# Kernel optimization log

Hardware: AMD Instinct MI355X
Metric: run time of the kernel (lower is better)

The kernel has to match this reference:

```python
import jax, jax.numpy as jnp
import numpy as np

KS = 3          # image feature patch kernel size
RATE = 2        # downsample rate; alpha patches use kernel RATE*2, stride RATE
PENALTY = -10000.0
EPS = 1e-4
BN_EPS = 1e-5


def _pad(x, k, s):
    # reflect 'same' padding as in GCAModule.pad
    l = (k - s + 1) // 2
    r = (k - s) // 2
    return jnp.pad(x, ((0, 0), (0, 0), (l, r), (l, r)), mode='reflect')


def _extract_patches(x, k, s):
    # replicates reflect-pad + F.unfold + reshape -> (n, L, c, k, k)
    x = _pad(x, k, s)
    n, c, H, W = x.shape
    oh = (H - k) // s + 1
    ow = (W - k) // s + 1
    cols = [x[:, :, di:di + s * (oh - 1) + 1:s, dj:dj + s * (ow - 1) + 1:s]
            for di in range(k) for dj in range(k)]
    p = jnp.stack(cols, axis=2).reshape(n, c, k, k, oh * ow)  # (n,c,k,k,L)
    return jnp.transpose(p, (0, 4, 1, 2, 3))                  # (n,L,c,k,k)


def _deconv(score, kern):
    # torch: F.conv_transpose2d(score[None], kern, stride=RATE, padding=1) / 4
    # score: (L,h,w); kern: (L, ac, 4, 4) in torch conv_transpose (I,O,kh,kw) layout
    k = jnp.transpose(jnp.flip(kern, axis=(2, 3)), (1, 0, 2, 3))  # -> OIHW
    out = jax.lax.conv_general_dilated(
        score[None], k, window_strides=(1, 1), padding=[(2, 2), (2, 2)],
        lhs_dilation=(RATE, RATE), dimension_numbers=('NCHW', 'OIHW', 'NCHW'))
    return out[0] / 4.0


def gca_forward(img_feat, alpha_feat, unknown, gconv_w, gconv_b, oconv_w,
                bn_gamma, bn_beta):
    n = img_feat.shape[0]
    # guidance 1x1 conv + nearest downsample by RATE
    g = jnp.einsum('nchw,oc->nohw', img_feat, gconv_w) + gconv_b[None, :, None, None]
    g = g[:, :, ::RATE, ::RATE]
    u = unknown[:, :, ::RATE, ::RATE]
    # process_unknown_mask: per-sample softmax scales
    um = u.mean(axis=(2, 3))                                    # (n,1)
    km = 1.0 - um
    unknown_scale = jnp.clip(jnp.sqrt(um / km), 0.1, 10.0)      # (n,1)
    known_scale = jnp.clip(jnp.sqrt(km / um), 0.1, 10.0)        # (n,1)
    h, w = g.shape[2], g.shape[3]
    L = h * w
    img_ps = _extract_patches(g, KS, 1)                         # (n,L,c,3,3)
    alpha_ps = _extract_patches(alpha_feat, RATE * 2, RATE)     # (n,L,ac,4,4)
    unk_ps = _extract_patches(u, KS, 1)[:, :, 0].mean(axis=(2, 3))  # (n,L)
    # l2-normalized image patch kernels
    norm = jnp.sqrt(jnp.sum(img_ps * img_ps, axis=(2, 3, 4), keepdims=True))
    img_ps_n = img_ps / jnp.maximum(norm, EPS)
    # similarity: conv of padded g with patch kernels == patches-at-p . kernel-q
    sim = jnp.einsum('npckl,nqckl->nqp', img_ps, img_ps_n)      # (n,L,L)
    is_unknown = (unk_ps > 0.0).astype(sim.dtype)               # (n,L)
    scale = unknown_scale * is_unknown + known_scale * (1.0 - is_unknown)
    out = sim * scale[:, :, None]
    idx = jnp.arange(L)
    out = out.at[:, idx, idx].add(PENALTY * unk_ps)             # self-corr penalty
    gca = jax.nn.softmax(out, axis=1).reshape(n, L, h, w)
    prop = jax.vmap(_deconv)(gca, alpha_ps)                     # (n,ac,2h,2w)
    # out_conv: 1x1 conv (no bias) + BatchNorm (training stats) + residual
    y = jnp.einsum('nchw,oc->nohw', prop, oconv_w)
    mu = y.mean(axis=(0, 2, 3), keepdims=True)
    var = y.var(axis=(0, 2, 3), keepdims=True)
    y = (y - mu) / jnp.sqrt(var + BN_EPS)
    y = y * bn_gamma[None, :, None, None] + bn_beta[None, :, None, None]
    return y + alpha_feat


def setup_inputs():
    key = jax.random.key(0)
    ks = jax.random.split(key, 8)
    N, C, AC, H, W = 4, 256, 128, 64, 64
    img_feat = jax.random.normal(ks[0], (N, C, H, W), jnp.float32)
    alpha_feat = jax.random.normal(ks[1], (N, AC, H, W), jnp.float32)
    unknown = jax.random.randint(ks[2], (N, 1, H, W), 0, 2).astype(jnp.float32)
    gconv_w = jax.random.normal(ks[3], (C // 2, C), jnp.float32) / np.float32(np.sqrt(C))
    gconv_b = jax.random.normal(ks[4], (C // 2,), jnp.float32) * 0.01
    oconv_w = jax.random.normal(ks[5], (AC, AC), jnp.float32) / np.float32(np.sqrt(AC))
    bn_gamma = 0.001 + jax.random.normal(ks[6], (AC,), jnp.float32) * 0.001
    bn_beta = jax.random.normal(ks[7], (AC,), jnp.float32) * 0.001
    return dict(img_feat=img_feat, alpha_feat=alpha_feat, unknown=unknown,
                gconv_w=gconv_w, gconv_b=gconv_b, oconv_w=oconv_w,
                bn_gamma=bn_gamma, bn_beta=bn_beta)


def reference(img_feat, alpha_feat, unknown, gconv_w, gconv_b, oconv_w,
              bn_gamma, bn_beta):
    return gca_forward(img_feat, alpha_feat, unknown, gconv_w, gconv_b,
                       oconv_w, bn_gamma, bn_beta)
```

## Files before the change

### kernel.cpp

```cpp
#include <hip/hip_runtime.h>

#define NN 4
#define CIN 256
#define CH 128
#define HH 64
#define hh 32
#define L 1024
#define NB 2048
#define PENALTY -10000.0f
#define EPS 1e-4f

typedef __bf16 bf16x8 __attribute__((ext_vector_type(8)));
typedef float f32x4 __attribute__((ext_vector_type(4)));
typedef __attribute__((address_space(3))) void lds_t;
typedef __attribute__((address_space(1))) const void gbl_t;

__device__ __forceinline__ int refl32(int t) { return t < 0 ? -t : (t > 31 ? 62 - t : t); }
__device__ __forceinline__ int refl64(int t) { return t < 0 ? -t : (t > 63 ? 126 - t : t); }
__device__ __forceinline__ int swz(int k, int row) { return k ^ (((row >> 1) & 3) << 3); }

__global__ void k_prep(const float* __restrict__ img, const float* __restrict__ gw,
                       const float* __restrict__ ow, const float* __restrict__ unknown,
                       const float* __restrict__ alpha,
                       __bf16* __restrict__ Xb, __bf16* __restrict__ gwb,
                       __bf16* __restrict__ owb, float* __restrict__ unk,
                       float* __restrict__ scales, __bf16* __restrict__ Bt,
                       float* __restrict__ stats) {
    __shared__ float sm[CIN * 33];
    int bid = blockIdx.x, t = threadIdx.x;
    if (bid < 512) {
        int n = bid >> 7, o = bid & 127;
        const float* ap = alpha + ((size_t)(n * CH + o) << 12);
#pragma unroll
        for (int j = 0; j < 4; ++j) {
            int fi = t + j * 256;
            int row = fi >> 4, c4 = fi & 15;
            float4 v = *(const float4*)(ap + fi * 4);
            float* d = sm + row * 65 + c4 * 4;
            d[0] = v.x; d[1] = v.y; d[2] = v.z; d[3] = v.w;
        }
        __syncthreads();
        __bf16* Bn = Bt + ((size_t)(n * NB) << 10);
#pragma unroll
        for (int gi = 0; gi < 8; ++gi) {
            int g = gi * 256 + t;
            int ab = g >> 7, qg = g & 127;
            int a = ab >> 2, bb = ab & 3;
            int q0 = qg * 8;
            int qi = q0 >> 5, qj0 = q0 & 31;
            int ti = refl64(2 * qi + a - 1);
            const float* r = sm + ti * 65;
            __bf16 v[8];
#pragma unroll
            for (int s = 0; s < 8; ++s) v[s] = (__bf16)r[refl64(2 * (qj0 + s) + bb - 1)];
            int j = ab * 128 + o;
            *(bf16x8*)(Bn + ((size_t)j << 10) + swz(q0, j)) = *(bf16x8*)v;
        }
    } else if (bid < 640) {
        int idx = bid - 512;
        int i = idx & 31, n = idx >> 5;
        for (int e = t; e < CIN * 32; e += 256) {
            int c = e >> 5, jj = e & 31;
            sm[c * 33 + jj] = img[(((size_t)n * CIN + c) * HH + 2 * i) * HH + 2 * jj];
        }
        __syncthreads();
#pragma unroll
        for (int j = 0; j < 32; ++j) {
            int np = (n << 10) + i * 32 + j;
            int cl = swz(t, np);
            Xb[(size_t)np * CIN + t] = (__bf16)sm[cl * 33 + j];
        }
    } else if (bid < 644) {
        int n = bid - 640;
        float* u = sm;
        float* red = sm + 1024;
        float part = 0.f;
#pragma unroll
        for (int c = 0; c < 4; ++c) {
            int idx = t + c * 256;
            int i = idx >> 5, j = idx & 31;
            float v = unknown[n * 4096 + (2 * i) * HH + 2 * j];
            u[idx] = v;
            part += v;
        }
        red[t] = part;
        __syncthreads();
        for (int s = 128; s > 0; s >>= 1) {
            if (t < s) red[t] += red[t + s];
            __syncthreads();
        }
        if (t == 0) {
            float um = red[0] / 1024.0f;
            float km = 1.0f - um;
            scales[n * 2] = fminf(fmaxf(sqrtf(um / km), 0.1f), 10.0f);
            scales[n * 2 + 1] = fminf(fmaxf(sqrtf(km / um), 0.1f), 10.0f);
        }
#pragma unroll
        for (int c = 0; c < 4; ++c) {
            int idx = t + c * 256;
            int i = idx >> 5, j = idx & 31;
            float sum = 0.f;
#pragma unroll
            for (int di = -1; di <= 1; ++di)
#pragma unroll
                for (int dj = -1; dj <= 1; ++dj)
                    sum += u[refl32(i + di) * 32 + refl32(j + dj)];
            unk[n * L + idx] = sum * (1.0f / 9.0f);
        }
    } else {
        if (bid == 644) stats[t] = 0.f;
        for (int e = (bid - 644) * 256 + t; e < 49152; e += 36 * 256) {
            if (e < 32768) {
                int o = e >> 8, m = e & 255;
                gwb[e] = (__bf16)gw[o * 256 + swz(m, o)];
            } else {
                int e2 = e - 32768;
                int j = e2 >> 7, m = e2 & 127;
                owb[e2] = (__bf16)ow[j * 128 + swz(m, j)];
            }
        }
    }
}

__global__ __launch_bounds__(256, 2) void k_gemm0(const __bf16* __restrict__ Xb,
                                                  const __bf16* __restrict__ gwb,
                                                  const float* __restrict__ gb,
                                                  __bf16* __restrict__ gbf) {
    __shared__ __align__(16) __bf16 As[128 * 32];
    __shared__ __align__(16) __bf16 Bs[128 * 32];
    int p0 = blockIdx.x * 128;
    int t = threadIdx.x, l = t & 63, w = t >> 6;
    int wr = w >> 1, wc = w & 1;
    f32x4 acc[4][4] = {};
    for (int k0 = 0; k0 < CIN; k0 += 32) {
#pragma unroll
        for (int i = 0; i < 2; ++i) {
            const __bf16* srcA = Xb + (size_t)(p0 + i * 64 + (t >> 2)) * CIN + k0 + (t & 3) * 8;
            __builtin_amdgcn_global_load_lds((gbl_t*)srcA, (lds_t*)(As + i * 2048 + t * 8), 16, 0, 0);
            const __bf16* srcB = gwb + (size_t)(i * 64 + (t >> 2)) * CIN + k0 + (t & 3) * 8;
            __builtin_amdgcn_global_load_lds((gbl_t*)srcB, (lds_t*)(Bs + i * 2048 + t * 8), 16, 0, 0);
        }
        __syncthreads();
        int gl = l >> 4, r = l & 15;
        bf16x8 av[4], bv[4];
#pragma unroll
        for (int m = 0; m < 4; ++m) {
            int row = wr * 64 + m * 16 + r;
            av[m] = *(const bf16x8*)(As + row * 32 + swz(gl << 3, row));
            int col = wc * 64 + m * 16 + r;
            bv[m] = *(const bf16x8*)(Bs + col * 32 + swz(gl << 3, col));
        }
#pragma unroll
        for (int m = 0; m < 4; ++m)
#pragma unroll
            for (int c2 = 0; c2 < 4; ++c2)
                acc[m][c2] = __builtin_amdgcn_mfma_f32_16x16x32_bf16(av[m], bv[c2], acc[m][c2], 0, 0, 0);
        __syncthreads();
    }
    int r = l & 15, hi = l >> 4;
#pragma unroll
    for (int m = 0; m < 4; ++m)
#pragma unroll
        for (int c2 = 0; c2 < 4; ++c2) {
            int o = wc * 64 + c2 * 16 + r;
            float bias = gb[o];
#pragma unroll
            for (int reg = 0; reg < 4; ++reg) {
                int row = p0 + wr * 64 + m * 16 + hi * 4 + reg;
                gbf[((size_t)row << 7) + o] = (__bf16)(acc[m][c2][reg] + bias);
            }
        }
}

__global__ __launch_bounds__(256, 2) void k_gemm1(const __bf16* __restrict__ gbf,
                                                  const float* __restrict__ unk,
                                                  const float* __restrict__ scales,
                                                  float* __restrict__ W) {
    __shared__ __align__(16) unsigned char RAW[75008];
    __bf16* As1 = (__bf16*)RAW;
    __bf16* Bh = (__bf16*)(RAW + 49152);
    float* ssq = (float*)(RAW + 73728);
    float* ftile = ssq + 192;
    int n = blockIdx.z;
    int p0 = blockIdx.y * 128, q0 = blockIdx.x * 128;
    const __bf16* gn = gbf + ((size_t)n << 17);
    int t = threadIdx.x, l = t & 63, w = t >> 6;
    int wr = w >> 1, wc = w & 1;
    int by4 = blockIdx.y * 4, bx4 = blockIdx.x * 4;
    int rbA = by4 - 1; rbA = rbA < 0 ? 0 : (rbA > 26 ? 26 : rbA);
    int rbB = bx4 - 1; rbB = rbB < 0 ? 0 : (rbB > 26 ? 26 : rbB);
#pragma unroll
    for (int k = 0; k < 12; ++k) {
        int chunk = k / 3;
        int rem = (k % 3) * 256 + t;
        int wrow = rem >> 2, sg = rem & 3;
        int so = (chunk << 5) + ((sg ^ ((wrow >> 1) & 3)) << 3);
        int grA = ((rbA + (wrow >> 5)) << 5) + (wrow & 31);
        __builtin_amdgcn_global_load_lds((gbl_t*)(gn + (size_t)grA * 128 + so),
                                         (lds_t*)(As1 + chunk * 6144 + rem * 8), 16, 0, 0);
    }
    auto stageB = [&](int h) {
#pragma unroll
        for (int k = 0; k < 6; ++k) {
            int cl = k / 3;
            int cc = 2 * h + cl;
            int rem = (k % 3) * 256 + t;
            int wrow = rem >> 2, sg = rem & 3;
            int so = (cc << 5) + ((sg ^ ((wrow >> 1) & 3)) << 3);
            int grB = ((rbB + (wrow >> 5)) << 5) + (wrow & 31);
            __builtin_amdgcn_global_load_lds((gbl_t*)(gn + (size_t)grB * 128 + so),
                                             (lds_t*)(Bh + cl * 6144 + rem * 8), 16, 0, 0);
        }
    };
    stageB(0);
    int gl = l >> 4, r = l & 15;
    int rpA_[4][3], cpA_[4][3], rpB_[4][3], cpB_[4][3];
#pragma unroll
    for (int m = 0; m < 4; ++m) {
        int prow = wr * 64 + m * 16 + r;
        int qrow = wc * 64 + m * 16 + r;
#pragma unroll
        for (int d = 0; d < 3; ++d) {
            rpA_[m][d] = (refl32(by4 + (prow >> 5) + d - 1) - rbA) << 10;
            int cp = refl32((prow & 31) + d - 1);
            cpA_[m][d] = cp * 32 + ((gl ^ ((cp >> 1) & 3)) << 3);
            rpB_[m][d] = (refl32(bx4 + (qrow >> 5) + d - 1) - rbB) << 10;
            int cq = refl32((qrow & 31) + d - 1);
            cpB_[m][d] = cq * 32 + ((gl ^ ((cq >> 1) & 3)) << 3);
        }
    }
    f32x4 acc[4][4] = {};
    float ssqAcc = 0.f;
    auto computeH = [&](int h) {
#pragma unroll
        for (int dk = 0; dk < 3; ++dk)
#pragma unroll
            for (int dl = 0; dl < 3; ++dl)
#pragma unroll
                for (int c = 0; c < 2; ++c) {
                    int cc = 2 * h + c;
                    bf16x8 av[4], bv[4];
#pragma unroll
                    for (int m = 0; m < 4; ++m) {
                        av[m] = *(const bf16x8*)(As1 + cc * 6144 + rpA_[m][dk] + cpA_[m][dl]);
                        bv[m] = *(const bf16x8*)(Bh + c * 6144 + rpB_[m][dk] + cpB_[m][dl]);
                    }
#pragma unroll
                    for (int m = 0; m < 4; ++m)
#pragma unroll
                        for (int c2 = 0; c2 < 4; ++c2)
                            acc[m][c2] = __builtin_amdgcn_mfma_f32_16x16x32_bf16(av[m], bv[c2], acc[m][c2], 0, 0, 0);
                }
        if (t < 192) {
            int key = (t >> 1) & 3;
#pragma unroll
            for (int c = 0; c < 2; ++c)
#pragma unroll
                for (int g = 0; g < 4; ++g) {
                    bf16x8 v = *(const bf16x8*)(Bh + c * 6144 + t * 32 + ((g ^ key) << 3));
#pragma unroll
                    for (int u2 = 0; u2 < 8; ++u2) {
                        float x = (float)v[u2];
                        ssqAcc += x * x;
                    }
                }
        }
    };
    __syncthreads();
    computeH(0);
    __syncthreads();
    stageB(1);
    __syncthreads();
    computeH(1);
    if (t < 192) ssq[t] = ssqAcc;
    __syncthreads();
    if (t < 128) {
        int q = q0 + t;
        int qi = q >> 5, qj = q & 31;
        float sum = 0.f;
#pragma unroll
        for (int di = -1; di <= 1; ++di)
#pragma unroll
            for (int dj = -1; dj <= 1; ++dj)
                sum += ssq[(refl32(qi + di) - rbB) * 32 + refl32(qj + dj)];
        float sc = unk[n * L + q] > 0.f ? scales[n * 2] : scales[n * 2 + 1];
        ftile[t] = sc / fmaxf(sqrtf(sum), EPS);
    }
    __syncthreads();
    int hi = l >> 4;
#pragma unroll
    for (int m = 0; m < 4; ++m)
#pragma unroll
        for (int c2 = 0; c2 < 4; ++c2) {
            int q = q0 + wc * 64 + c2 * 16 + r;
            float fq = ftile[wc * 64 + c2 * 16 + r];
#pragma unroll
            for (int reg = 0; reg < 4; ++reg) {
                int p = p0 + wr * 64 + m * 16 + hi * 4 + reg;
                float val = acc[m][c2][reg] * fq;
                if (p == q) val += PENALTY * unk[n * L + p];
                W[((size_t)n << 20) + ((size_t)p << 10) + q] = val;
            }
        }
}

__global__ void k_softmax(const float* __restrict__ W, __bf16* __restrict__ Wb) {
    int t = threadIdx.x, wv = t >> 6, lane = t & 63;
    int row = blockIdx.x * 4 + wv;
    const float* Wr = W + (size_t)row * 1024;
    float v[16];
    float mx = -1e30f;
#pragma unroll
    for (int k = 0; k < 16; ++k) {
        v[k] = Wr[lane + k * 64];
        mx = fmaxf(mx, v[k]);
    }
#pragma unroll
    for (int off = 32; off > 0; off >>= 1) mx = fmaxf(mx, __shfl_xor(mx, off));
    float sum = 0.f;
#pragma unroll
    for (int k = 0; k < 16; ++k) {
        v[k] = __expf(v[k] - mx);
        sum += v[k];
    }
#pragma unroll
    for (int off = 32; off > 0; off >>= 1) sum += __shfl_xor(sum, off);
    float inv = 1.0f / sum;
    int p = row & (L - 1);
    int key = ((p >> 1) & 3) << 3;
    __bf16* Wbr = Wb + (size_t)row * 1024;
#pragma unroll
    for (int k = 0; k < 16; ++k) {
        int idx = lane + k * 64;
        Wbr[idx ^ key] = (__bf16)(v[k] * inv);
    }
}

__global__ __launch_bounds__(256, 2) void k_gemm2(const __bf16* __restrict__ Wb,
                                                  const __bf16* __restrict__ Bt,
                                                  __bf16* __restrict__ Tb) {
    int bid = blockIdx.x;
    int xcd = bid & 7, idx = bid >> 3;
    int n = xcd >> 1;
    int p0 = ((xcd & 1) * 4 + (idx & 3)) * 128;
    int j0 = (idx >> 2) * 128;
    __shared__ __align__(16) __bf16 As[4][4096];
    __shared__ __align__(16) __bf16 Bs[4][4096];
    const __bf16* An = Wb + ((size_t)n << 20);
    const __bf16* Bn = Bt + ((size_t)n * NB << 10);
    int t = threadIdx.x, l = t & 63, w = t >> 6;
    int wr = w >> 1, wc = w & 1;
    int gl = l >> 4, r = l & 15;
    f32x4 acc[4][4] = {};

    auto stage = [&](int buf, int k0) {
#pragma unroll
        for (int i = 0; i < 2; ++i) {
            int row = (t >> 2) + i * 64;
            int sgo = (t & 3) * 8;
            const __bf16* srcA = An + ((size_t)(p0 + row) << 10) + k0 + sgo;
            __builtin_amdgcn_global_load_lds((gbl_t*)srcA, (lds_t*)(&As[buf][row * 32 + sgo]), 16, 0, 0);
            const __bf16* srcB = Bn + ((size_t)(j0 + row) << 10) + k0 + sgo;
            __builtin_amdgcn_global_load_lds((gbl_t*)srcB, (lds_t*)(&Bs[buf][row * 32 + sgo]), 16, 0, 0);
        }
    };
    auto compute = [&](int buf) {
        bf16x8 av[4], bv[4];
#pragma unroll
        for (int m = 0; m < 4; ++m) {
            int row = wr * 64 + m * 16 + r;
            av[m] = *(const bf16x8*)(&As[buf][row * 32 + ((gl ^ ((row >> 1) & 3)) << 3)]);
            int col = wc * 64 + m * 16 + r;
            bv[m] = *(const bf16x8*)(&Bs[buf][col * 32 + ((gl ^ ((col >> 1) & 3)) << 3)]);
        }
#pragma unroll
        for (int m = 0; m < 4; ++m)
#pragma unroll
            for (int c2 = 0; c2 < 4; ++c2)
                acc[m][c2] = __builtin_amdgcn_mfma_f32_16x16x32_bf16(av[m], bv[c2], acc[m][c2], 0, 0, 0);
    };

    stage(0, 0);
    stage(1, 32);
    for (int it = 0; it < 32; ++it) {
        int buf = it & 3;
        if (it + 2 < 32) stage((it + 2) & 3, (it + 2) * 32);
        if (it < 30)
            asm volatile("s_waitcnt vmcnt(8)\n\ts_barrier" ::: "memory");
        else if (it == 30)
            asm volatile("s_waitcnt vmcnt(4)\n\ts_barrier" ::: "memory");
        else
            asm volatile("s_waitcnt vmcnt(0)\n\ts_barrier" ::: "memory");
        compute(buf);
    }
    int hi = l >> 4;
#pragma unroll
    for (int m = 0; m < 4; ++m)
#pragma unroll
        for (int c2 = 0; c2 < 4; ++c2) {
            int j = j0 + wc * 64 + c2 * 16 + r;
#pragma unroll
            for (int reg = 0; reg < 4; ++reg) {
                int p = p0 + wr * 64 + m * 16 + hi * 4 + reg;
                Tb[((size_t)n * L + p) * NB + j] = (__bf16)acc[m][c2][reg];
            }
        }
}

__global__ void k_oconv(const __bf16* __restrict__ owb, const __bf16* __restrict__ Tb,
                        float* __restrict__ y2, float* __restrict__ stats) {
    __shared__ __align__(16) __bf16 As[4 * 4096];
    __shared__ __align__(16) __bf16 Bp[4 * 2048];
    int n = blockIdx.z;
    int x0 = blockIdx.x * 64;
    int t = threadIdx.x, l = t & 63, w = t >> 6;
    int wr = w >> 1, wc = w & 1;
    int gl = l >> 4, r = l & 15, hi = l >> 4;
#pragma unroll
    for (int c = 0; c < 4; ++c)
#pragma unroll
        for (int i = 0; i < 2; ++i) {
            int h = i * 256 + t;
            const __bf16* src = owb + (size_t)(h >> 2) * CH + c * 32 + (h & 3) * 8;
            __builtin_amdgcn_global_load_lds((gbl_t*)src, (lds_t*)(As + c * 4096 + h * 8), 16, 0, 0);
        }
    const __bf16* Tn = Tb + ((size_t)(n * L) << 11);
#pragma unroll
    for (int it = 0; it < 4; ++it) {
        int e2 = it * 256 + t;
        int og = e2 & 15, pl = e2 >> 4;
        int pix = x0 + pl;
        int x = pix & 63, y = pix >> 6;
        float acc8[8] = {};
        int ap = (y + 1) & 1, bp = (x + 1) & 1;
#pragma unroll
        for (int da = 0; da < 2; ++da) {
            int a = ap + 2 * da;
            int ny = y + 1 - a;
            if (ny < 0 || ny >= 64) continue;
            int py = ny >> 1;
#pragma unroll
            for (int db = 0; db < 2; ++db) {
                int bb = bp + 2 * db;
                int nx = x + 1 - bb;
                if (nx < 0 || nx >= 64) continue;
                int px = nx >> 1;
                bf16x8 v = *(const bf16x8*)(Tn + (((size_t)(py * hh + px)) << 11) + (a * 4 + bb) * 128 + og * 8);
#pragma unroll
                for (int u2 = 0; u2 < 8; ++u2) acc8[u2] += (float)v[u2];
            }
        }
        __bf16 rr[8];
#pragma unroll
        for (int u2 = 0; u2 < 8; ++u2) rr[u2] = (__bf16)(acc8[u2] * 0.25f);
        int key = (pix >> 1) & 3;
        int dgl = (og & 3) ^ key;
        *(bf16x8*)(Bp + (og >> 2) * 2048 + pl * 32 + dgl * 8) = *(bf16x8*)rr;
    }
    __syncthreads();
    f32x4 acc[4][2] = {};
#pragma unroll
    for (int c = 0; c < 4; ++c) {
        bf16x8 av[4], bv[2];
#pragma unroll
        for (int m = 0; m < 4; ++m) {
            int row = wr * 64 + m * 16 + r;
            av[m] = *(const bf16x8*)(As + c * 4096 + row * 32 + ((gl ^ ((row >> 1) & 3)) << 3));
        }
#pragma unroll
        for (int c2 = 0; c2 < 2; ++c2) {
            int col = wc * 32 + c2 * 16 + r;
            bv[c2] = *(const bf16x8*)(Bp + c * 2048 + col * 32 + ((gl ^ ((col >> 1) & 3)) << 3));
        }
#pragma unroll
        for (int m = 0; m < 4; ++m)
#pragma unroll
            for (int c2 = 0; c2 < 2; ++c2)
                acc[m][c2] = __builtin_amdgcn_mfma_f32_16x16x32_bf16(av[m], bv[c2], acc[m][c2], 0, 0, 0);
    }
#pragma unroll
    for (int m = 0; m < 4; ++m)
#pragma unroll
        for (int c2 = 0; c2 < 2; ++c2) {
            int pix = x0 + wc * 32 + c2 * 16 + r;
#pragma unroll
            for (int reg = 0; reg < 4; ++reg) {
                int j = wr * 64 + m * 16 + hi * 4 + reg;
                y2[(((size_t)n * CH + j) << 12) + pix] = acc[m][c2][reg];
            }
        }
    __syncthreads();
    float* partS = (float*)As;
    float* partS2 = partS + 256;
#pragma unroll
    for (int m = 0; m < 4; ++m)
#pragma unroll
        for (int reg = 0; reg < 4; ++reg) {
            float s = 0.f, s2 = 0.f;
#pragma unroll
            for (int c2 = 0; c2 < 2; ++c2) {
                float v = acc[m][c2][reg];
                s += v;
                s2 += v * v;
            }
#pragma unroll
            for (int off = 1; off < 16; off <<= 1) {
                s += __shfl_xor(s, off);
                s2 += __shfl_xor(s2, off);
            }
            if (r == 0) {
                int j = wr * 64 + m * 16 + hi * 4 + reg;
                partS[j * 2 + wc] = s;
                partS2[j * 2 + wc] = s2;
            }
        }
    __syncthreads();
    if (t < 128) {
        atomicAdd(&stats[t * 2], partS[t * 2] + partS[t * 2 + 1]);
        atomicAdd(&stats[t * 2 + 1], partS2[t * 2] + partS2[t * 2 + 1]);
    }
}

__global__ void k_final(const float* __restrict__ y2, const float* __restrict__ stats,
                        const float* __restrict__ gamma, const float* __restrict__ beta,
                        const float* __restrict__ alpha, float* __restrict__ out) {
    int e4 = blockIdx.x * 256 + threadIdx.x;
    int oc = (e4 >> 10) & 127;
    float s1 = stats[oc * 2], s2 = stats[oc * 2 + 1];
    float mu = s1 * (1.0f / 16384.0f);
    float var = s2 * (1.0f / 16384.0f) - mu * mu;
    float inv = rsqrtf(var + 1e-5f);
    float g = gamma[oc], b = beta[oc];
    float4 yv = ((const float4*)y2)[e4];
    float4 av = ((const float4*)alpha)[e4];
    float4 o;
    o.x = (yv.x - mu) * inv * g + b + av.x;
    o.y = (yv.y - mu) * inv * g + b + av.y;
    o.z = (yv.z - mu) * inv * g + b + av.z;
    o.w = (yv.w - mu) * inv * g + b + av.w;
    ((float4*)out)[e4] = o;
}

extern "C" void kernel_launch(void* const* d_in, const int* in_sizes, int n_in,
                              void* d_out, int out_size, void* d_ws, size_t ws_size,
                              hipStream_t stream) {
    const float* img = (const float*)d_in[0];
    const float* alpha = (const float*)d_in[1];
    const float* unknown = (const float*)d_in[2];
    const float* gw = (const float*)d_in[3];
    const float* gb = (const float*)d_in[4];
    const float* ow = (const float*)d_in[5];
    const float* gamma = (const float*)d_in[6];
    const float* beta = (const float*)d_in[7];
    float* out = (float*)d_out;
    float* ws = (float*)d_ws;

    __bf16* Xb = (__bf16*)(ws);
    __bf16* gwb = (__bf16*)(ws + 524288);
    __bf16* owb = (__bf16*)(ws + 540672);
    __bf16* gbf = (__bf16*)(ws + 548864);
    float* unk = ws + 815104;
    float* scales = ws + 819200;
    float* stats = ws + 819264;
    float* W = ws + 819520;
    __bf16* Wb = (__bf16*)(ws + 5013824);
    __bf16* Bt = (__bf16*)(ws + 7110976);
    __bf16* Tb = (__bf16*)(ws + 11305280);
    float* y2 = ws + 15499584;

    k_prep<<<680, 256, 0, stream>>>(img, gw, ow, unknown, alpha, Xb, gwb, owb, unk, scales, Bt, stats);
    k_gemm0<<<32, 256, 0, stream>>>(Xb, gwb, gb, gbf);
    k_gemm1<<<dim3(8, 8, 4), 256, 0, stream>>>(gbf, unk, scales, W);
    k_softmax<<<1024, 256, 0, stream>>>(W, Wb);
    k_gemm2<<<512, 256, 0, stream>>>(Wb, Bt, Tb);
    k_oconv<<<dim3(64, 1, 4), 256, 0, stream>>>(owb, Tb, y2, stats);
    k_final<<<2048, 256, 0, stream>>>(y2, stats, gamma, beta, alpha, out);
}
```

Before: 92.65 us.

## Fuse batchnorm finalize into oconv via grid-wide barrier; vectorize image downsample loads

The output-conv kernel now waits at a software grid barrier (an atomic counter spin) after accumulating BN statistics. It then applies normalization and the residual add directly from registers, so the separate final kernel and the y2 round trip through global memory are gone. The counter is reset in the prep kernel. The prep kernel's strided downsample of img now uses float4 loads, and gemm1's MFMA section raises wave priority. The grid barrier relies on all 256 blocks being co-resident, and could deadlock if they are not.

```diff
diff --git a/kernel.cpp b/kernel.cpp
--- a/kernel.cpp
+++ b/kernel.cpp
@@ -59,9 +59,11 @@
     } else if (bid < 640) {
         int idx = bid - 512;
         int i = idx & 31, n = idx >> 5;
-        for (int e = t; e < CIN * 32; e += 256) {
-            int c = e >> 5, jj = e & 31;
-            sm[c * 33 + jj] = img[(((size_t)n * CIN + c) * HH + 2 * i) * HH + 2 * jj];
+        for (int e = t; e < CIN * 16; e += 256) {
+            int c = e >> 4, j2 = e & 15;
+            float4 v = *(const float4*)(img + (((size_t)n * CIN + c) * HH + 2 * i) * HH + 4 * j2);
+            sm[c * 33 + 2 * j2] = v.x;
+            sm[c * 33 + 2 * j2 + 1] = v.z;
         }
         __syncthreads();
 #pragma unroll
@@ -108,7 +110,10 @@
             unk[n * L + idx] = sum * (1.0f / 9.0f);
         }
     } else {
-        if (bid == 644) stats[t] = 0.f;
+        if (bid == 644) {
+            stats[t] = 0.f;
+            if (t == 0) *(unsigned*)(scales + 56) = 0u;
+        }
         for (int e = (bid - 644) * 256 + t; e < 49152; e += 36 * 256) {
             if (e < 32768) {
                 int o = e >> 8, m = e & 255;
@@ -232,6 +237,7 @@
     f32x4 acc[4][4] = {};
     float ssqAcc = 0.f;
     auto computeH = [&](int h) {
+        __builtin_amdgcn_s_setprio(1);
 #pragma unroll
         for (int dk = 0; dk < 3; ++dk)
 #pragma unroll
@@ -251,6 +257,7 @@
                         for (int c2 = 0; c2 < 4; ++c2)
                             acc[m][c2] = __builtin_amdgcn_mfma_f32_16x16x32_bf16(av[m], bv[c2], acc[m][c2], 0, 0, 0);
                 }
+        __builtin_amdgcn_s_setprio(0);
         if (t < 192) {
             int key = (t >> 1) & 3;
 #pragma unroll
@@ -408,7 +415,9 @@
 }
 
 __global__ void k_oconv(const __bf16* __restrict__ owb, const __bf16* __restrict__ Tb,
-                        float* __restrict__ y2, float* __restrict__ stats) {
+                        float* __restrict__ stats, const float* __restrict__ gamma,
+                        const float* __restrict__ beta, const float* __restrict__ alpha,
+                        float* __restrict__ out, unsigned* __restrict__ flags) {
     __shared__ __align__(16) __bf16 As[4 * 4096];
     __shared__ __align__(16) __bf16 Bp[4 * 2048];
     int n = blockIdx.z;
@@ -478,17 +487,6 @@
             for (int c2 = 0; c2 < 2; ++c2)
                 acc[m][c2] = __builtin_amdgcn_mfma_f32_16x16x32_bf16(av[m], bv[c2], acc[m][c2], 0, 0, 0);
     }
-#pragma unroll
-    for (int m = 0; m < 4; ++m)
-#pragma unroll
-        for (int c2 = 0; c2 < 2; ++c2) {
-            int pix = x0 + wc * 32 + c2 * 16 + r;
-#pragma unroll
-            for (int reg = 0; reg < 4; ++reg) {
-                int j = wr * 64 + m * 16 + hi * 4 + reg;
-                y2[(((size_t)n * CH + j) << 12) + pix] = acc[m][c2][reg];
-            }
-        }
     __syncthreads();
     float* partS = (float*)As;
     float* partS2 = partS + 256;
@@ -519,26 +517,38 @@
         atomicAdd(&stats[t * 2], partS[t * 2] + partS[t * 2 + 1]);
         atomicAdd(&stats[t * 2 + 1], partS2[t * 2] + partS2[t * 2 + 1]);
     }
-}
-
-__global__ void k_final(const float* __restrict__ y2, const float* __restrict__ stats,
-                        const float* __restrict__ gamma, const float* __restrict__ beta,
-                        const float* __restrict__ alpha, float* __restrict__ out) {
-    int e4 = blockIdx.x * 256 + threadIdx.x;
-    int oc = (e4 >> 10) & 127;
-    float s1 = stats[oc * 2], s2 = stats[oc * 2 + 1];
-    float mu = s1 * (1.0f / 16384.0f);
-    float var = s2 * (1.0f / 16384.0f) - mu * mu;
-    float inv = rsqrtf(var + 1e-5f);
-    float g = gamma[oc], b = beta[oc];
-    float4 yv = ((const float4*)y2)[e4];
-    float4 av = ((const float4*)alpha)[e4];
-    float4 o;
-    o.x = (yv.x - mu) * inv * g + b + av.x;
-    o.y = (yv.y - mu) * inv * g + b + av.y;
-    o.z = (yv.z - mu) * inv * g + b + av.z;
-    o.w = (yv.w - mu) * inv * g + b + av.w;
-    ((float4*)out)[e4] = o;
+    __syncthreads();
+    if (t == 0) {
+        __threadfence();
+        atomicAdd(flags, 1u);
+        while (atomicAdd(flags, 0u) < 256u) __builtin_amdgcn_s_sleep(1);
+    }
+    __syncthreads();
+    float* mu_s = (float*)Bp;
+    float* ivg_s = mu_s + 128;
+    float* bt_s = mu_s + 256;
+    if (t < 128) {
+        float s1 = atomicAdd(&stats[t * 2], 0.0f);
+        float s2 = atomicAdd(&stats[t * 2 + 1], 0.0f);
+        float mu = s1 * (1.0f / 16384.0f);
+        float var = s2 * (1.0f / 16384.0f) - mu * mu;
+        mu_s[t] = mu;
+        ivg_s[t] = rsqrtf(var + 1e-5f) * gamma[t];
+        bt_s[t] = beta[t];
+    }
+    __syncthreads();
+#pragma unroll
+    for (int m = 0; m < 4; ++m)
+#pragma unroll
+        for (int c2 = 0; c2 < 2; ++c2) {
+            int pix = x0 + wc * 32 + c2 * 16 + r;
+#pragma unroll
+            for (int reg = 0; reg < 4; ++reg) {
+                int j = wr * 64 + m * 16 + hi * 4 + reg;
+                size_t off = (((size_t)n * CH + j) << 12) + pix;
+                out[off] = (acc[m][c2][reg] - mu_s[j]) * ivg_s[j] + bt_s[j] + alpha[off];
+            }
+        }
 }
 
 extern "C" void kernel_launch(void* const* d_in, const int* in_sizes, int n_in,
@@ -566,13 +576,12 @@
     __bf16* Wb = (__bf16*)(ws + 5013824);
     __bf16* Bt = (__bf16*)(ws + 7110976);
     __bf16* Tb = (__bf16*)(ws + 11305280);
-    float* y2 = ws + 15499584;
+    unsigned* flags = (unsigned*)(ws + 819256);
 
     k_prep<<<680, 256, 0, stream>>>(img, gw, ow, unknown, alpha, Xb, gwb, owb, unk, scales, Bt, stats);
     k_gemm0<<<32, 256, 0, stream>>>(Xb, gwb, gb, gbf);
     k_gemm1<<<dim3(8, 8, 4), 256, 0, stream>>>(gbf, unk, scales, W);
     k_softmax<<<1024, 256, 0, stream>>>(W, Wb);
     k_gemm2<<<512, 256, 0, stream>>>(Wb, Bt, Tb);
-    k_oconv<<<dim3(64, 1, 4), 256, 0, stream>>>(owb, Tb, y2, stats);
-    k_final<<<2048, 256, 0, stream>>>(y2, stats, gamma, beta, alpha, out);
-}
+    k_oconv<<<dim3(64, 1, 4), 256, 0, stream>>>(owb, Tb, stats, gamma, beta, alpha, out, flags);
+}
```

Result: slower. 108.3 us (+16.9%).

## Move alpha patch transpose into gemm1 launch to overlap with correlation GEMM

Applied to the files above, without the earlier changes.

The alpha-feature patch extraction into Bt moves out of k_prep and into extra blocks of k_gemm1. That gemm1 launch becomes a 1D grid of 768 blocks, 256 of them doing the GEMM, so the memory-bound transpose can overlap the compute-bound correlation GEMM and k_prep gets shorter ahead of gemm0. The image downsample load now uses float4 reads and keeps every other element, and MFMA sections raise wave priority with s_setprio. Risk: the extra blocks share the 75 KB LDS allocation, which may limit co-residency or delay GEMM blocks.

```diff
diff --git a/kernel.cpp b/kernel.cpp
--- a/kernel.cpp
+++ b/kernel.cpp
@@ -21,47 +21,18 @@
 
 __global__ void k_prep(const float* __restrict__ img, const float* __restrict__ gw,
                        const float* __restrict__ ow, const float* __restrict__ unknown,
-                       const float* __restrict__ alpha,
                        __bf16* __restrict__ Xb, __bf16* __restrict__ gwb,
                        __bf16* __restrict__ owb, float* __restrict__ unk,
-                       float* __restrict__ scales, __bf16* __restrict__ Bt,
-                       float* __restrict__ stats) {
+                       float* __restrict__ scales, float* __restrict__ stats) {
     __shared__ float sm[CIN * 33];
     int bid = blockIdx.x, t = threadIdx.x;
-    if (bid < 512) {
-        int n = bid >> 7, o = bid & 127;
-        const float* ap = alpha + ((size_t)(n * CH + o) << 12);
-#pragma unroll
-        for (int j = 0; j < 4; ++j) {
-            int fi = t + j * 256;
-            int row = fi >> 4, c4 = fi & 15;
-            float4 v = *(const float4*)(ap + fi * 4);
-            float* d = sm + row * 65 + c4 * 4;
-            d[0] = v.x; d[1] = v.y; d[2] = v.z; d[3] = v.w;
-        }
-        __syncthreads();
-        __bf16* Bn = Bt + ((size_t)(n * NB) << 10);
-#pragma unroll
-        for (int gi = 0; gi < 8; ++gi) {
-            int g = gi * 256 + t;
-            int ab = g >> 7, qg = g & 127;
-            int a = ab >> 2, bb = ab & 3;
-            int q0 = qg * 8;
-            int qi = q0 >> 5, qj0 = q0 & 31;
-            int ti = refl64(2 * qi + a - 1);
-            const float* r = sm + ti * 65;
-            __bf16 v[8];
-#pragma unroll
-            for (int s = 0; s < 8; ++s) v[s] = (__bf16)r[refl64(2 * (qj0 + s) + bb - 1)];
-            int j = ab * 128 + o;
-            *(bf16x8*)(Bn + ((size_t)j << 10) + swz(q0, j)) = *(bf16x8*)v;
-        }
-    } else if (bid < 640) {
-        int idx = bid - 512;
-        int i = idx & 31, n = idx >> 5;
-        for (int e = t; e < CIN * 32; e += 256) {
-            int c = e >> 5, jj = e & 31;
-            sm[c * 33 + jj] = img[(((size_t)n * CIN + c) * HH + 2 * i) * HH + 2 * jj];
+    if (bid < 128) {
+        int i = bid & 31, n = bid >> 5;
+        for (int e = t; e < CIN * 16; e += 256) {
+            int c = e >> 4, j2 = e & 15;
+            float4 v = *(const float4*)(img + (((size_t)n * CIN + c) * HH + 2 * i) * HH + 4 * j2);
+            sm[c * 33 + 2 * j2] = v.x;
+            sm[c * 33 + 2 * j2 + 1] = v.z;
         }
         __syncthreads();
 #pragma unroll
@@ -70,8 +41,8 @@
             int cl = swz(t, np);
             Xb[(size_t)np * CIN + t] = (__bf16)sm[cl * 33 + j];
         }
-    } else if (bid < 644) {
-        int n = bid - 640;
+    } else if (bid < 132) {
+        int n = bid - 128;
         float* u = sm;
         float* red = sm + 1024;
         float part = 0.f;
@@ -108,8 +79,8 @@
             unk[n * L + idx] = sum * (1.0f / 9.0f);
         }
     } else {
-        if (bid == 644) stats[t] = 0.f;
-        for (int e = (bid - 644) * 256 + t; e < 49152; e += 36 * 256) {
+        if (bid == 132) stats[t] = 0.f;
+        for (int e = (bid - 132) * 256 + t; e < 49152; e += 36 * 256) {
             if (e < 32768) {
                 int o = e >> 8, m = e & 255;
                 gwb[e] = (__bf16)gw[o * 256 + swz(m, o)];
@@ -175,18 +146,54 @@
 __global__ __launch_bounds__(256, 2) void k_gemm1(const __bf16* __restrict__ gbf,
                                                   const float* __restrict__ unk,
                                                   const float* __restrict__ scales,
-                                                  float* __restrict__ W) {
+                                                  const float* __restrict__ alpha,
+                                                  float* __restrict__ W,
+                                                  __bf16* __restrict__ Bt) {
     __shared__ __align__(16) unsigned char RAW[75008];
+    int bid = blockIdx.x, t = threadIdx.x;
+    if (bid >= 256) {
+        float* sm = (float*)RAW;
+        int blk = bid - 256;
+        int n = blk >> 7, o = blk & 127;
+        const float* ap = alpha + ((size_t)(n * CH + o) << 12);
+#pragma unroll
+        for (int j = 0; j < 4; ++j) {
+            int fi = t + j * 256;
+            int row = fi >> 4, c4 = fi & 15;
+            float4 v = *(const float4*)(ap + fi * 4);
+            float* d = sm + row * 65 + c4 * 4;
+            d[0] = v.x; d[1] = v.y; d[2] = v.z; d[3] = v.w;
+        }
+        __syncthreads();
+        __bf16* Bn = Bt + ((size_t)(n * NB) << 10);
+#pragma unroll
+        for (int gi = 0; gi < 8; ++gi) {
+            int g = gi * 256 + t;
+            int ab = g >> 7, qg = g & 127;
+            int a = ab >> 2, bb = ab & 3;
+            int q0 = qg * 8;
+            int qi = q0 >> 5, qj0 = q0 & 31;
+            int ti = refl64(2 * qi + a - 1);
+            const float* r = sm + ti * 65;
+            __bf16 v[8];
+#pragma unroll
+            for (int s = 0; s < 8; ++s) v[s] = (__bf16)r[refl64(2 * (qj0 + s) + bb - 1)];
+            int j = ab * 128 + o;
+            *(bf16x8*)(Bn + ((size_t)j << 10) + swz(q0, j)) = *(bf16x8*)v;
+        }
+        return;
+    }
     __bf16* As1 = (__bf16*)RAW;
     __bf16* Bh = (__bf16*)(RAW + 49152);
     float* ssq = (float*)(RAW + 73728);
     float* ftile = ssq + 192;
-    int n = blockIdx.z;
-    int p0 = blockIdx.y * 128, q0 = blockIdx.x * 128;
+    int n = bid >> 6;
+    int yy = (bid >> 3) & 7, xx = bid & 7;
+    int p0 = yy * 128, q0 = xx * 128;
     const __bf16* gn = gbf + ((size_t)n << 17);
-    int t = threadIdx.x, l = t & 63, w = t >> 6;
+    int l = t & 63, w = t >> 6;
     int wr = w >> 1, wc = w & 1;
-    int by4 = blockIdx.y * 4, bx4 = blockIdx.x * 4;
+    int by4 = yy * 4, bx4 = xx * 4;
     int rbA = by4 - 1; rbA = rbA < 0 ? 0 : (rbA > 26 ? 26 : rbA);
     int rbB = bx4 - 1; rbB = rbB < 0 ? 0 : (rbB > 26 ? 26 : rbB);
 #pragma unroll
@@ -232,6 +239,7 @@
     f32x4 acc[4][4] = {};
     float ssqAcc = 0.f;
     auto computeH = [&](int h) {
+        __builtin_amdgcn_s_setprio(1);
 #pragma unroll
         for (int dk = 0; dk < 3; ++dk)
 #pragma unroll
@@ -251,6 +259,7 @@
                         for (int c2 = 0; c2 < 4; ++c2)
                             acc[m][c2] = __builtin_amdgcn_mfma_f32_16x16x32_bf16(av[m], bv[c2], acc[m][c2], 0, 0, 0);
                 }
+        __builtin_amdgcn_s_setprio(0);
         if (t < 192) {
             int key = (t >> 1) & 3;
 #pragma unroll
@@ -568,9 +577,9 @@
     __bf16* Tb = (__bf16*)(ws + 11305280);
     float* y2 = ws + 15499584;
 
-    k_prep<<<680, 256, 0, stream>>>(img, gw, ow, unknown, alpha, Xb, gwb, owb, unk, scales, Bt, stats);
+    k_prep<<<168, 256, 0, stream>>>(img, gw, ow, unknown, Xb, gwb, owb, unk, scales, stats);
     k_gemm0<<<32, 256, 0, stream>>>(Xb, gwb, gb, gbf);
-    k_gemm1<<<dim3(8, 8, 4), 256, 0, stream>>>(gbf, unk, scales, W);
+    k_gemm1<<<768, 256, 0, stream>>>(gbf, unk, scales, alpha, W, Bt);
     k_softmax<<<1024, 256, 0, stream>>>(W, Wb);
     k_gemm2<<<512, 256, 0, stream>>>(Wb, Bt, Tb);
     k_oconv<<<dim3(64, 1, 4), 256, 0, stream>>>(owb, Tb, y2, stats);
```

Result: no change. 91.26 us (-1.5%).
